# Optimization experiments

Measured on AMD Instinct MI355X. Metric: run time of the kernel, lower is better.

## Reference

```python
import jax, jax.numpy as jnp
import numpy as np

N_NODES = 50000
N_EDGES = 800000
NFEAT, NHID, NHEAD, NCLASS = 512, 64, 8, 40
NEG_SLOPE = 0.2  # LeakyReLU alpha from __init__


def setup_inputs() -> dict:
    key = jax.random.key(0)
    ks = jax.random.split(key, 8)
    glorot = lambda k, shape: jax.random.normal(k, shape, jnp.float32) * (2.0 / (shape[-2] + shape[-1])) ** 0.5
    return {
        "x": jax.random.normal(ks[0], (N_NODES, NFEAT), jnp.float32),
        "edge_list": jax.random.randint(ks[1], (2, N_EDGES), 0, N_NODES, jnp.int32),
        # nhead input-layer GATconv params: weight [H, nfeat, nhid], att [H, 2*nhid], bias [H, nhid]
        "W1": glorot(ks[2], (NHEAD, NFEAT, NHID)),
        "a1": jax.random.normal(ks[3], (NHEAD, 2 * NHID), jnp.float32) * 0.1,
        "b1": jnp.zeros((NHEAD, NHID), jnp.float32),
        # single output-head GATconv: [nhid*nhead, nclass]
        "W2": glorot(ks[4], (NHEAD * NHID, NCLASS)),
        "a2": jax.random.normal(ks[5], (2 * NCLASS,), jnp.float32) * 0.1,
        "b2": jnp.zeros((NCLASS,), jnp.float32),
    }


def _gat_layer(x, W, a, b, src, dst, n_nodes):
    """One GATconv head (eval mode, dropout = identity)."""
    h = x @ W                                  # [N, F]
    f = W.shape[-1]
    s_src = h @ a[:f]                          # [N] per-node src score
    s_dst = h @ a[f:]                          # [N] per-node dst score
    e = jax.nn.leaky_relu(s_src[src] + s_dst[dst], NEG_SLOPE)  # [E]
    # segment softmax over incoming edges of each dst node (numerically stable)
    m = jax.ops.segment_max(e, dst, num_segments=n_nodes)
    m = jax.lax.stop_gradient(jnp.where(jnp.isfinite(m), m, 0.0))
    w = jnp.exp(e - m[dst])
    denom = jax.ops.segment_sum(w, dst, num_segments=n_nodes)
    alpha = w / jnp.maximum(denom[dst], 1e-16)                 # [E]
    out = jax.ops.segment_sum(alpha[:, None] * h[src], dst, num_segments=n_nodes)
    return out + b


def reference(x, edge_list, W1, a1, b1, W2, a2, b2):
    n = x.shape[0]
    src, dst = edge_list[0], edge_list[1]
    # multi-head input layer, concat along feature dim
    heads = jax.vmap(lambda W, a, b: _gat_layer(x, W, a, b, src, dst, n))(W1, a1, b1)  # [H, N, nhid]
    h = jax.nn.elu(jnp.transpose(heads, (1, 0, 2)).reshape(n, -1))                      # [N, H*nhid]
    # single output head (mean over nhead_out=1)
    out = _gat_layer(h, W2, a2, b2, src, dst, n)                                        # [N, nclass]
    return jax.nn.log_softmax(out, axis=1)
```

## Files before the change

### kernel.cpp

```cpp
#include <hip/hip_runtime.h>
#include <math.h>

#define N_NODES 50000
#define N_EDGES 800000
#define NFEAT 512
#define NHID 64
#define NHEAD 8
#define NCLASS 40
#define NEG_SLOPE 0.2f

#define N_RT 3125
#define N_RT_PAD 3128
#define SCAN_NBLK 49

typedef __attribute__((ext_vector_type(8))) short short8;
typedef __attribute__((ext_vector_type(4))) short short4v;
typedef __attribute__((ext_vector_type(4))) float f32x4;

__device__ __forceinline__ float bf2f(short s) {
    return __uint_as_float(((unsigned)(unsigned short)s) << 16);
}
__device__ __forceinline__ short f2bf(float f) {
    unsigned u = __float_as_uint(f);
    unsigned r = (u + 0x7FFFu + ((u >> 16) & 1u)) >> 16;
    return (short)(unsigned short)r;
}



__global__ void count_deg(const int* __restrict__ el, int* __restrict__ deg) {
    int e = blockIdx.x * blockDim.x + threadIdx.x;
    if (e < N_EDGES) atomicAdd(&deg[el[N_EDGES + e]], 1);
}

__global__ __launch_bounds__(256) void scan1(const int* __restrict__ deg,
                                             int* __restrict__ loc,
                                             int* __restrict__ bsum) {
    int tid = threadIdx.x, lane = tid & 63, w = tid >> 6;
    int base = blockIdx.x * 1024 + tid * 4;
    int d0 = (base + 0 < N_NODES) ? deg[base + 0] : 0;
    int d1 = (base + 1 < N_NODES) ? deg[base + 1] : 0;
    int d2 = (base + 2 < N_NODES) ? deg[base + 2] : 0;
    int d3 = (base + 3 < N_NODES) ? deg[base + 3] : 0;
    int s0 = d0, s1 = s0 + d1, s2 = s1 + d2, s3 = s2 + d3;
    int t = s3;
#pragma unroll
    for (int d = 1; d < 64; d <<= 1) {
        int u = __shfl_up(t, d);
        if (lane >= d) t += u;
    }
    __shared__ int wsum[4];
    if (lane == 63) wsum[w] = t;
    __syncthreads();
    int woff = 0;
#pragma unroll
    for (int j = 0; j < 4; ++j) woff += (j < w) ? wsum[j] : 0;
    int excl = woff + t - s3;
    if (base + 0 < N_NODES) loc[base + 0] = excl + s0;
    if (base + 1 < N_NODES) loc[base + 1] = excl + s1;
    if (base + 2 < N_NODES) loc[base + 2] = excl + s2;
    if (base + 3 < N_NODES) loc[base + 3] = excl + s3;
    if (tid == 255) bsum[blockIdx.x] = woff + t;
}

__global__ __launch_bounds__(256) void scan3(const int* __restrict__ deg,
                                             const int* __restrict__ loc,
                                             const int* __restrict__ bsum,
                                             int* __restrict__ ptr,
                                             int* __restrict__ cursor) {
    __shared__ int sOff;
    if (threadIdx.x < 64) {
        int lane = threadIdx.x;
        int v = (lane < SCAN_NBLK && lane < (int)blockIdx.x) ? bsum[lane] : 0;
#pragma unroll
        for (int m = 1; m < 64; m <<= 1) v += __shfl_xor(v, m);
        if (lane == 0) sOff = v;
    }
    __syncthreads();
    int off = sOff;
    int base = blockIdx.x * 1024 + threadIdx.x * 4;
    if (blockIdx.x == 0 && threadIdx.x == 0) ptr[0] = 0;
#pragma unroll
    for (int k = 0; k < 4; ++k) {
        int i = base + k;
        if (i < N_NODES) {
            int P = off + loc[i];
            ptr[i + 1] = P;
            cursor[i] = P - deg[i];
        }
    }
}

__global__ void scatter_k(const int* __restrict__ el, int* __restrict__ cursor,
                          int* __restrict__ esrc) {
    int e = blockIdx.x * blockDim.x + threadIdx.x;
    if (e >= N_EDGES) return;
    int dst = el[N_EDGES + e];
    int p = atomicAdd(&cursor[dst], 1);
    esrc[p] = el[e];
}

__global__ __launch_bounds__(256) void pack_w(const float* __restrict__ W1,
                                              const float* __restrict__ W2,
                                              short* __restrict__ Wp1,
                                              short* __restrict__ Wp2) {
    int t = blockIdx.x * 256 + threadIdx.x;
    if (t < 32768) {
        int l = t & 63, ct = (t >> 6) & 7, ks = (t >> 9) & 15, g = t >> 13;
        int c = g * 128 + ct * 16 + (l & 15);
        int head = c >> 6, f = c & 63;
        int k0 = ks * 32 + (l >> 4) * 8;
        short8 o;
#pragma unroll
        for (int j = 0; j < 8; ++j)
            o[j] = f2bf(W1[(size_t)head * NFEAT * NHID + (k0 + j) * NHID + f]);
        *(short8*)(Wp1 + (size_t)t * 8) = o;
    } else if (t < 32768 + 3072) {
        int u = t - 32768;
        int l = u & 63;
        int kc = u >> 6;
        int ct2 = kc % 3, ks = kc / 3;
        int col = ct2 * 16 + (l & 15);
        short8 o;
#pragma unroll
        for (int j = 0; j < 8; ++j) {
            int kp = ks * 32 + (l >> 4) * 8 + j;
            int head = kp >> 6, fp = kp & 63;
            int l15 = fp >> 2, ctp = fp & 3;
            int ct = ((head & 1) << 2) | ctp;
            int gg = head >> 1;
            int orig_k = gg * 128 + ct * 16 + l15;
            o[j] = (col < NCLASS) ? f2bf(W2[(size_t)orig_k * NCLASS + col]) : (short)0;
        }
        *(short8*)(Wp2 + (size_t)u * 8) = o;
    }
}

__global__ __launch_bounds__(256, 2) void gemm1(const float* __restrict__ x,
                                                const short* __restrict__ Wp1,
                                                const float* __restrict__ a1,
                                                short* __restrict__ h1p,
                                                float* __restrict__ s1s,
                                                float* __restrict__ s1d) {
    __shared__ short As[2 * 16 * 64 * 8];
    int w = threadIdx.x >> 6, l = threadIdx.x & 63;
    int g = w;
    int rt0 = blockIdx.x * 2;
    int row0 = rt0 * 16;

#pragma unroll
    for (int u = 0; u < 8; ++u) {
        int idx = threadIdx.x + u * 256;
        int rl = idx >> 6, cg = idx & 63;
        int row = row0 + rl;
        short8 o;
        if (row < N_NODES) {
            const float* p = x + (size_t)row * NFEAT + cg * 8;
            float4 v0 = *(const float4*)p;
            float4 v1 = *(const float4*)(p + 4);
            o[0] = f2bf(v0.x); o[1] = f2bf(v0.y); o[2] = f2bf(v0.z); o[3] = f2bf(v0.w);
            o[4] = f2bf(v1.x); o[5] = f2bf(v1.y); o[6] = f2bf(v1.z); o[7] = f2bf(v1.w);
        } else {
#pragma unroll
            for (int j = 0; j < 8; ++j) o[j] = 0;
        }
        int rtl = rl >> 4, rloc = rl & 15, ks = cg >> 2, sub = cg & 3;
        int lane = rloc + sub * 16;
        *(short8*)(As + (((rtl * 16 + ks) * 64) + lane) * 8) = o;
    }
    __syncthreads();

    f32x4 acc[2][8];
#pragma unroll
    for (int i = 0; i < 2; ++i)
#pragma unroll
        for (int ct = 0; ct < 8; ++ct) acc[i][ct] = (f32x4){0.f, 0.f, 0.f, 0.f};

    const short* bP = Wp1 + (size_t)g * 16 * 4096 + l * 8;
    short8 bc[8];
#pragma unroll
    for (int ct = 0; ct < 8; ++ct) bc[ct] = *(const short8*)(bP + ct * 512);

    for (int ks = 0; ks < 16; ++ks) {
        int kn = (ks < 15) ? ks + 1 : ks;
        short8 bn[8];
#pragma unroll
        for (int ct = 0; ct < 8; ++ct) bn[ct] = *(const short8*)(bP + kn * 4096 + ct * 512);
        short8 a0 = *(const short8*)(As + ((ks)*64 + l) * 8);
        short8 a1v = *(const short8*)(As + ((16 + ks) * 64 + l) * 8);
#pragma unroll
        for (int ct = 0; ct < 8; ++ct) {
            acc[0][ct] = __builtin_amdgcn_mfma_f32_16x16x32_bf16(a0, bc[ct], acc[0][ct], 0, 0, 0);
            acc[1][ct] = __builtin_amdgcn_mfma_f32_16x16x32_bf16(a1v, bc[ct], acc[1][ct], 0, 0, 0);
        }
#pragma unroll
        for (int ct = 0; ct < 8; ++ct) bc[ct] = bn[ct];
    }

    float avs[8], avd[8];
#pragma unroll
    for (int ct = 0; ct < 8; ++ct) {
        int head = 2 * g + (ct >> 2);
        int f = (ct & 3) * 16 + (l & 15);
        avs[ct] = a1[head * 128 + f];
        avd[ct] = a1[head * 128 + 64 + f];
    }
    int l15 = l & 15;
    int rbase = (l >> 4) * 4;
#pragma unroll
    for (int i = 0; i < 2; ++i)
#pragma unroll
        for (int r = 0; r < 4; ++r) {
            int row = (rt0 + i) * 16 + rbase + r;
            float ps0 = 0.f, pd0 = 0.f, ps1 = 0.f, pd1 = 0.f;
#pragma unroll
            for (int ct = 0; ct < 4; ++ct) {
                ps0 += acc[i][ct][r] * avs[ct];
                pd0 += acc[i][ct][r] * avd[ct];
            }
#pragma unroll
            for (int ct = 4; ct < 8; ++ct) {
                ps1 += acc[i][ct][r] * avs[ct];
                pd1 += acc[i][ct][r] * avd[ct];
            }
#pragma unroll
            for (int mask = 1; mask < 16; mask <<= 1) {
                ps0 += __shfl_xor(ps0, mask);
                pd0 += __shfl_xor(pd0, mask);
                ps1 += __shfl_xor(ps1, mask);
                pd1 += __shfl_xor(pd1, mask);
            }
            if (row < N_NODES) {
                if (l15 == 0) {
                    s1s[row * 8 + 2 * g]     = ps0;
                    s1d[row * 8 + 2 * g]     = pd0;
                    s1s[row * 8 + 2 * g + 1] = ps1;
                    s1d[row * 8 + 2 * g + 1] = pd1;
                }
                short4v o0, o1;
#pragma unroll
                for (int c = 0; c < 4; ++c) { o0[c] = f2bf(acc[i][c][r]); o1[c] = f2bf(acc[i][4 + c][r]); }
                size_t base = (size_t)row * 512 + g * 128 + l15 * 4;
                *(short4v*)(h1p + base) = o0;
                *(short4v*)(h1p + base + 64) = o1;
            }
        }
}

__global__ __launch_bounds__(256, 4) void att1(const int* __restrict__ ptr,
                                               const int* __restrict__ esrc,
                                               const float* __restrict__ s1s,
                                               const float* __restrict__ s1d,
                                               const short* __restrict__ h1p,
                                               const float* __restrict__ b1,
                                               short* __restrict__ hcat) {
    int n = blockIdx.x * 4 + (threadIdx.x >> 6);
    int l = threadIdx.x & 63;
    if (n >= N_NODES) return;
    int beg = ptr[n], end = ptr[n + 1];
    int h = l >> 3;
    float sd = s1d[n * 8 + h];
    float den = 0.f;
    float acc[8] = {0.f, 0.f, 0.f, 0.f, 0.f, 0.f, 0.f, 0.f};
    const short* hb = h1p + l * 8;
    if (beg < end) {
        int last = end - 1;
        int p1 = (beg + 1 <= last) ? beg + 1 : last;
        int p2 = (beg + 2 <= last) ? beg + 2 : last;
        int p3 = (beg + 3 <= last) ? beg + 3 : last;
        int s0 = esrc[beg], s1 = esrc[p1], s2 = esrc[p2], s3 = esrc[p3];
        short8 v0 = *(const short8*)(hb + (size_t)s0 * 512);
        short8 v1 = *(const short8*)(hb + (size_t)s1 * 512);
        short8 v2 = *(const short8*)(hb + (size_t)s2 * 512);
        short8 v3 = *(const short8*)(hb + (size_t)s3 * 512);
        float ss0 = s1s[s0 * 8 + h], ss1 = s1s[s1 * 8 + h];
        float ss2 = s1s[s2 * 8 + h], ss3 = s1s[s3 * 8 + h];
        for (int i = beg; i < end; i += 4) {
            int ni = i + 4;
            int t0 = s0, t1 = s1, t2 = s2, t3 = s3;
            short8 u0 = v0, u1 = v1, u2 = v2, u3 = v3;
            float ts0 = ss0, ts1 = ss1, ts2 = ss2, ts3 = ss3;
            if (ni < end) {
                int q1 = (ni + 1 <= last) ? ni + 1 : last;
                int q2 = (ni + 2 <= last) ? ni + 2 : last;
                int q3 = (ni + 3 <= last) ? ni + 3 : last;
                t0 = esrc[ni]; t1 = esrc[q1]; t2 = esrc[q2]; t3 = esrc[q3];
                u0 = *(const short8*)(hb + (size_t)t0 * 512);
                u1 = *(const short8*)(hb + (size_t)t1 * 512);
                u2 = *(const short8*)(hb + (size_t)t2 * 512);
                u3 = *(const short8*)(hb + (size_t)t3 * 512);
                ts0 = s1s[t0 * 8 + h]; ts1 = s1s[t1 * 8 + h];
                ts2 = s1s[t2 * 8 + h]; ts3 = s1s[t3 * 8 + h];
            }
            float e0 = ss0 + sd, e1 = ss1 + sd, e2 = ss2 + sd, e3 = ss3 + sd;
            e0 = fmaxf(e0, NEG_SLOPE * e0);
            e1 = fmaxf(e1, NEG_SLOPE * e1);
            e2 = fmaxf(e2, NEG_SLOPE * e2);
            e3 = fmaxf(e3, NEG_SLOPE * e3);
            float w0 = __expf(e0);
            float w1 = (i + 1 < end) ? __expf(e1) : 0.f;
            float w2 = (i + 2 < end) ? __expf(e2) : 0.f;
            float w3 = (i + 3 < end) ? __expf(e3) : 0.f;
            den += (w0 + w1) + (w2 + w3);
#pragma unroll
            for (int j = 0; j < 8; ++j)
                acc[j] += (w0 * bf2f(v0[j]) + w1 * bf2f(v1[j])) +
                          (w2 * bf2f(v2[j]) + w3 * bf2f(v3[j]));
            s0 = t0; s1 = t1; s2 = t2; s3 = t3;
            v0 = u0; v1 = u1; v2 = u2; v3 = u3;
            ss0 = ts0; ss1 = ts1; ss2 = ts2; ss3 = ts3;
        }
    }
    float rden = 1.f / fmaxf(den, 1e-16f);
    short8 o;
#pragma unroll
    for (int j = 0; j < 8; ++j) {
        int forig = (j & 3) * 16 + (l & 7) * 2 + (j >> 2);
        float v = acc[j] * rden + b1[h * 64 + forig];
        v = v > 0.f ? v : (__expf(v) - 1.f);
        o[j] = f2bf(v);
    }
    *(short8*)(hcat + (size_t)n * 512 + l * 8) = o;
}

__global__ __launch_bounds__(256) void gemm2(const short* __restrict__ hcat,
                                             const short* __restrict__ Wp2,
                                             const float* __restrict__ a2,
                                             short* __restrict__ h2,
                                             float* __restrict__ s2s,
                                             float* __restrict__ s2d) {
    int w = threadIdx.x >> 6, l = threadIdx.x & 63;
    int rt = blockIdx.x * 4 + w;
    int arow = rt * 16 + (l & 15);
    const short* aBase = hcat + (size_t)arow * 512 + (l >> 4) * 8;
    f32x4 acc[3];
#pragma unroll
    for (int ct = 0; ct < 3; ++ct) acc[ct] = (f32x4){0.f, 0.f, 0.f, 0.f};
#pragma unroll 2
    for (int ks = 0; ks < 16; ++ks) {
        short8 a = *(const short8*)(aBase + ks * 32);
        const short* bp = Wp2 + (size_t)(ks * 3) * 512 + l * 8;
#pragma unroll
        for (int ct = 0; ct < 3; ++ct) {
            short8 b = *(const short8*)(bp + ct * 512);
            acc[ct] = __builtin_amdgcn_mfma_f32_16x16x32_bf16(a, b, acc[ct], 0, 0, 0);
        }
    }
    float ps[4] = {0.f, 0.f, 0.f, 0.f}, pd[4] = {0.f, 0.f, 0.f, 0.f};
    int cl = l & 15, rb = (l >> 4) * 4;
#pragma unroll
    for (int ct = 0; ct < 3; ++ct) {
        int col = ct * 16 + cl;
        if (col < NCLASS) {
#pragma unroll
            for (int r = 0; r < 4; ++r) {
                ps[r] += acc[ct][r] * a2[col];
                pd[r] += acc[ct][r] * a2[NCLASS + col];
                int row = rt * 16 + rb + r;
                if (row < N_NODES) h2[(size_t)row * NCLASS + col] = f2bf(acc[ct][r]);
            }
        }
    }
#pragma unroll
    for (int mask = 1; mask < 16; mask <<= 1)
#pragma unroll
        for (int r = 0; r < 4; ++r) {
            ps[r] += __shfl_xor(ps[r], mask);
            pd[r] += __shfl_xor(pd[r], mask);
        }
    if (cl == 0) {
#pragma unroll
        for (int r = 0; r < 4; ++r) {
            int row = rt * 16 + rb + r;
            if (row < N_NODES) { s2s[row] = ps[r]; s2d[row] = pd[r]; }
        }
    }
}

__global__ __launch_bounds__(256, 4) void att2(const int* __restrict__ ptr,
                                               const int* __restrict__ esrc,
                                               const float* __restrict__ s2s,
                                               const float* __restrict__ s2d,
                                               const short* __restrict__ h2,
                                               const float* __restrict__ b2,
                                               float* __restrict__ out) {
    int n = blockIdx.x * 4 + (threadIdx.x >> 6);
    int l = threadIdx.x & 63;
    if (n >= N_NODES) return;
    int beg = ptr[n], end = ptr[n + 1];
    float sd = s2d[n];
    float den = 0.f, acc = 0.f;
    int last = end - 1;
    bool act = (l < NCLASS);
    for (int i = beg; i < end; i += 4) {
        int i1 = (i + 1 <= last) ? i + 1 : last;
        int i2 = (i + 2 <= last) ? i + 2 : last;
        int i3 = (i + 3 <= last) ? i + 3 : last;
        int s0 = esrc[i], s1 = esrc[i1], s2 = esrc[i2], s3 = esrc[i3];
        float h0 = act ? bf2f(h2[(size_t)s0 * NCLASS + l]) : 0.f;
        float h1 = act ? bf2f(h2[(size_t)s1 * NCLASS + l]) : 0.f;
        float hh2 = act ? bf2f(h2[(size_t)s2 * NCLASS + l]) : 0.f;
        float h3 = act ? bf2f(h2[(size_t)s3 * NCLASS + l]) : 0.f;
        float e0 = s2s[s0] + sd;
        float e1 = s2s[s1] + sd;
        float e2 = s2s[s2] + sd;
        float e3 = s2s[s3] + sd;
        e0 = fmaxf(e0, NEG_SLOPE * e0);
        e1 = fmaxf(e1, NEG_SLOPE * e1);
        e2 = fmaxf(e2, NEG_SLOPE * e2);
        e3 = fmaxf(e3, NEG_SLOPE * e3);
        float w0 = __expf(e0);
        float w1 = (i + 1 < end) ? __expf(e1) : 0.f;
        float w2 = (i + 2 < end) ? __expf(e2) : 0.f;
        float w3 = (i + 3 < end) ? __expf(e3) : 0.f;
        den += (w0 + w1) + (w2 + w3);
        acc += (w0 * h0 + w1 * h1) + (w2 * hh2 + w3 * h3);
    }
    float v = act ? acc / fmaxf(den, 1e-16f) + b2[l] : -INFINITY;
    float mx = v;
#pragma unroll
    for (int o = 32; o; o >>= 1) mx = fmaxf(mx, __shfl_down(mx, o));
    mx = __shfl(mx, 0);
    float ex = act ? __expf(v - mx) : 0.f;
    float s = ex;
#pragma unroll
    for (int o = 32; o; o >>= 1) s += __shfl_down(s, o);
    s = __shfl(s, 0);
    float ls = __logf(s);
    if (act) out[(size_t)n * NCLASS + l] = v - mx - ls;
}


extern "C" void kernel_launch(void* const* d_in, const int* in_sizes, int n_in,
                              void* d_out, int out_size, void* d_ws, size_t ws_size,
                              hipStream_t stream) {
    const float* x  = (const float*)d_in[0];
    const int*   el = (const int*)d_in[1];
    const float* W1 = (const float*)d_in[2];
    const float* a1 = (const float*)d_in[3];
    const float* b1 = (const float*)d_in[4];
    const float* W2 = (const float*)d_in[5];
    const float* a2 = (const float*)d_in[6];
    const float* b2 = (const float*)d_in[7];
    float* out = (float*)d_out;

    short* sbase = (short*)d_ws;
    short* hcat  = sbase + 25624576;
    short* h1p   = sbase + 51249152;
    short* Wp1   = sbase + 76849152;
    short* Wp2   = sbase + 77111296;
    short* h2    = sbase + 77135872;
    float* fbase = (float*)(sbase + 79135872);
    float* s1s   = fbase;
    float* s1d   = fbase + 400000;
    float* s2s   = fbase + 800000;
    float* s2d   = fbase + 850000;
    int*   ibase = (int*)(fbase + 900000);
    int*   deg    = ibase;
    int*   ptr    = ibase + 50000;
    int*   cursor = ibase + 100001;
    int*   esrc   = ibase + 150001;
    int*   loc    = ibase + 950001;
    int*   bsum   = ibase + 1000001;

    hipMemsetAsync(deg, 0, (size_t)N_NODES * 4, stream);
    count_deg<<<(N_EDGES + 255) / 256, 256, 0, stream>>>(el, deg);
    scan1<<<SCAN_NBLK, 256, 0, stream>>>(deg, loc, bsum);
    scan3<<<SCAN_NBLK, 256, 0, stream>>>(deg, loc, bsum, ptr, cursor);
    scatter_k<<<(N_EDGES + 255) / 256, 256, 0, stream>>>(el, cursor, esrc);

    pack_w<<<140, 256, 0, stream>>>(W1, W2, Wp1, Wp2);

    gemm1<<<N_RT_PAD / 2, 256, 0, stream>>>(x, Wp1, a1, h1p, s1s, s1d);
    att1<<<(N_NODES + 3) / 4, 256, 0, stream>>>(ptr, esrc, s1s, s1d, h1p, b1, hcat);

    gemm2<<<N_RT_PAD / 4, 256, 0, stream>>>(hcat, Wp2, a2, h2, s2s, s2d);
    att2<<<(N_NODES + 3) / 4, 256, 0, stream>>>(ptr, esrc, s2s, s2d, h2, b2, out);
}
```

Measured before the change: 533.7 us.

## Deepen weight prefetch to two k-steps, swizzle LDS tile, nontemporal x loads

The first-layer projection GEMM now prefetches B fragments two k-steps ahead instead of one, processing k in pairs so more global loads are in flight across MFMAs. The LDS A-tile uses an XOR swizzle on slot indices to reduce bank conflicts on the short8 stores and loads. The x input is read with nontemporal loads since it is streamed once. The deeper prefetch doubles the B register footprint, which may raise VGPR pressure and lower occupancy.

```diff
diff --git a/kernel.cpp b/kernel.cpp
--- a/kernel.cpp
+++ b/kernel.cpp
@@ -25,6 +25,7 @@
     unsigned r = (u + 0x7FFFu + ((u >> 16) & 1u)) >> 16;
     return (short)(unsigned short)r;
 }
+__device__ __forceinline__ int swz(int s) { return s ^ ((s >> 4) & 7); }
 
 
 
@@ -156,17 +157,18 @@
         short8 o;
         if (row < N_NODES) {
             const float* p = x + (size_t)row * NFEAT + cg * 8;
-            float4 v0 = *(const float4*)p;
-            float4 v1 = *(const float4*)(p + 4);
-            o[0] = f2bf(v0.x); o[1] = f2bf(v0.y); o[2] = f2bf(v0.z); o[3] = f2bf(v0.w);
-            o[4] = f2bf(v1.x); o[5] = f2bf(v1.y); o[6] = f2bf(v1.z); o[7] = f2bf(v1.w);
+            f32x4 v0 = __builtin_nontemporal_load((const f32x4*)p);
+            f32x4 v1 = __builtin_nontemporal_load((const f32x4*)(p + 4));
+            o[0] = f2bf(v0[0]); o[1] = f2bf(v0[1]); o[2] = f2bf(v0[2]); o[3] = f2bf(v0[3]);
+            o[4] = f2bf(v1[0]); o[5] = f2bf(v1[1]); o[6] = f2bf(v1[2]); o[7] = f2bf(v1[3]);
         } else {
 #pragma unroll
             for (int j = 0; j < 8; ++j) o[j] = 0;
         }
         int rtl = rl >> 4, rloc = rl & 15, ks = cg >> 2, sub = cg & 3;
         int lane = rloc + sub * 16;
-        *(short8*)(As + (((rtl * 16 + ks) * 64) + lane) * 8) = o;
+        int slot = (rtl * 16 + ks) * 64 + lane;
+        *(short8*)(As + swz(slot) * 8) = o;
     }
     __syncthreads();
 
@@ -177,24 +179,37 @@
         for (int ct = 0; ct < 8; ++ct) acc[i][ct] = (f32x4){0.f, 0.f, 0.f, 0.f};
 
     const short* bP = Wp1 + (size_t)g * 16 * 4096 + l * 8;
-    short8 bc[8];
-#pragma unroll
-    for (int ct = 0; ct < 8; ++ct) bc[ct] = *(const short8*)(bP + ct * 512);
-
-    for (int ks = 0; ks < 16; ++ks) {
-        int kn = (ks < 15) ? ks + 1 : ks;
-        short8 bn[8];
-#pragma unroll
-        for (int ct = 0; ct < 8; ++ct) bn[ct] = *(const short8*)(bP + kn * 4096 + ct * 512);
-        short8 a0 = *(const short8*)(As + ((ks)*64 + l) * 8);
-        short8 a1v = *(const short8*)(As + ((16 + ks) * 64 + l) * 8);
+    short8 b0[8], b1[8], n0[8], n1[8];
+#pragma unroll
+    for (int ct = 0; ct < 8; ++ct) b0[ct] = *(const short8*)(bP + ct * 512);
+#pragma unroll
+    for (int ct = 0; ct < 8; ++ct) b1[ct] = *(const short8*)(bP + 4096 + ct * 512);
+
+    for (int kk = 0; kk < 8; ++kk) {
+        int ks0 = 2 * kk, ks1 = 2 * kk + 1;
+        int kp0 = (ks0 + 2 < 16) ? ks0 + 2 : 15;
+        int kp1 = (ks1 + 2 < 16) ? ks1 + 2 : 15;
+#pragma unroll
+        for (int ct = 0; ct < 8; ++ct) n0[ct] = *(const short8*)(bP + kp0 * 4096 + ct * 512);
+#pragma unroll
+        for (int ct = 0; ct < 8; ++ct) n1[ct] = *(const short8*)(bP + kp1 * 4096 + ct * 512);
+
+        short8 a00 = *(const short8*)(As + swz(ks0 * 64 + l) * 8);
+        short8 a01 = *(const short8*)(As + swz((16 + ks0) * 64 + l) * 8);
 #pragma unroll
         for (int ct = 0; ct < 8; ++ct) {
-            acc[0][ct] = __builtin_amdgcn_mfma_f32_16x16x32_bf16(a0, bc[ct], acc[0][ct], 0, 0, 0);
-            acc[1][ct] = __builtin_amdgcn_mfma_f32_16x16x32_bf16(a1v, bc[ct], acc[1][ct], 0, 0, 0);
-        }
-#pragma unroll
-        for (int ct = 0; ct < 8; ++ct) bc[ct] = bn[ct];
+            acc[0][ct] = __builtin_amdgcn_mfma_f32_16x16x32_bf16(a00, b0[ct], acc[0][ct], 0, 0, 0);
+            acc[1][ct] = __builtin_amdgcn_mfma_f32_16x16x32_bf16(a01, b0[ct], acc[1][ct], 0, 0, 0);
+        }
+        short8 a10 = *(const short8*)(As + swz(ks1 * 64 + l) * 8);
+        short8 a11 = *(const short8*)(As + swz((16 + ks1) * 64 + l) * 8);
+#pragma unroll
+        for (int ct = 0; ct < 8; ++ct) {
+            acc[0][ct] = __builtin_amdgcn_mfma_f32_16x16x32_bf16(a10, b1[ct], acc[0][ct], 0, 0, 0);
+            acc[1][ct] = __builtin_amdgcn_mfma_f32_16x16x32_bf16(a11, b1[ct], acc[1][ct], 0, 0, 0);
+        }
+#pragma unroll
+        for (int ct = 0; ct < 8; ++ct) { b0[ct] = n0[ct]; b1[ct] = n1[ct]; }
     }
 
     float avs[8], avd[8];
```

Measured after the change: 522.6 us. 1.02x faster.

## Fold attention vectors into W1 as extra GEMM column tile, enlarge gemm1 row tile

Applied to the files above, without the earlier changes.

Precomputes W1·a_src and W1·a_dst per head and packs them as a ninth 16-wide column tile, so gemm1 produces the attention scores directly from the MFMA instead of doing a shuffle-reduction epilogue. gemm1 also now processes 4 row tiles per block instead of 2, applies an XOR swizzle to the LDS A layout, and uses nontemporal loads for x. The B-operand prefetch double-buffering is removed in favor of unroll 2. The scores are now computed from bf16-rounded projected weights, which slightly changes numerics, and the larger accumulator array raises register pressure.

```diff
diff --git a/kernel.cpp b/kernel.cpp
--- a/kernel.cpp
+++ b/kernel.cpp
@@ -12,6 +12,7 @@
 #define N_RT 3125
 #define N_RT_PAD 3128
 #define SCAN_NBLK 49
+#define RT_BLK 4
 
 typedef __attribute__((ext_vector_type(8))) short short8;
 typedef __attribute__((ext_vector_type(4))) short short4v;
@@ -25,6 +26,7 @@
     unsigned r = (u + 0x7FFFu + ((u >> 16) & 1u)) >> 16;
     return (short)(unsigned short)r;
 }
+__device__ __forceinline__ int swz(int s) { return s ^ ((s >> 4) & 7); }
 
 
 
@@ -102,21 +104,45 @@
 
 __global__ __launch_bounds__(256) void pack_w(const float* __restrict__ W1,
                                               const float* __restrict__ W2,
-                                              short* __restrict__ Wp1,
+                                              const float* __restrict__ a1,
+                                              short* __restrict__ Wp1a,
                                               short* __restrict__ Wp2) {
     int t = blockIdx.x * 256 + threadIdx.x;
-    if (t < 32768) {
-        int l = t & 63, ct = (t >> 6) & 7, ks = (t >> 9) & 15, g = t >> 13;
-        int c = g * 128 + ct * 16 + (l & 15);
-        int head = c >> 6, f = c & 63;
-        int k0 = ks * 32 + (l >> 4) * 8;
+    if (t < 36864) {
+        int l = t & 63;
+        int idx = t >> 6;
+        int ct = idx % 9;
+        int ksg = idx / 9;
+        int ks = ksg & 15, g = ksg >> 4;
         short8 o;
-#pragma unroll
-        for (int j = 0; j < 8; ++j)
-            o[j] = f2bf(W1[(size_t)head * NFEAT * NHID + (k0 + j) * NHID + f]);
-        *(short8*)(Wp1 + (size_t)t * 8) = o;
-    } else if (t < 32768 + 3072) {
-        int u = t - 32768;
+        if (ct < 8) {
+            int c = g * 128 + ct * 16 + (l & 15);
+            int head = c >> 6, f = c & 63;
+            int k0 = ks * 32 + (l >> 4) * 8;
+#pragma unroll
+            for (int j = 0; j < 8; ++j)
+                o[j] = f2bf(W1[(size_t)head * NFEAT * NHID + (k0 + j) * NHID + f]);
+        } else {
+            int col = l & 15;
+            int k0 = ks * 32 + (l >> 4) * 8;
+#pragma unroll
+            for (int j = 0; j < 8; ++j) o[j] = 0;
+            if (col < 4) {
+                int head = 2 * g + (col >> 1);
+                const float* av = a1 + head * 128 + (col & 1) * 64;
+                const float* wb = W1 + (size_t)head * NFEAT * NHID;
+#pragma unroll
+                for (int j = 0; j < 8; ++j) {
+                    const float* wr = wb + (size_t)(k0 + j) * NHID;
+                    float s = 0.f;
+                    for (int f = 0; f < NHID; ++f) s += wr[f] * av[f];
+                    o[j] = f2bf(s);
+                }
+            }
+        }
+        *(short8*)(Wp1a + (size_t)t * 8) = o;
+    } else if (t < 36864 + 3072) {
+        int u = t - 36864;
         int l = u & 63;
         int kc = u >> 6;
         int ct2 = kc % 3, ks = kc / 3;
@@ -137,112 +163,80 @@
 }
 
 __global__ __launch_bounds__(256, 2) void gemm1(const float* __restrict__ x,
-                                                const short* __restrict__ Wp1,
-                                                const float* __restrict__ a1,
+                                                const short* __restrict__ Wp1a,
                                                 short* __restrict__ h1p,
                                                 float* __restrict__ s1s,
                                                 float* __restrict__ s1d) {
-    __shared__ short As[2 * 16 * 64 * 8];
+    __shared__ short As[RT_BLK * 16 * 64 * 8];
     int w = threadIdx.x >> 6, l = threadIdx.x & 63;
     int g = w;
-    int rt0 = blockIdx.x * 2;
+    int rt0 = blockIdx.x * RT_BLK;
     int row0 = rt0 * 16;
 
 #pragma unroll
-    for (int u = 0; u < 8; ++u) {
+    for (int u = 0; u < 4 * RT_BLK; ++u) {
         int idx = threadIdx.x + u * 256;
         int rl = idx >> 6, cg = idx & 63;
         int row = row0 + rl;
         short8 o;
         if (row < N_NODES) {
             const float* p = x + (size_t)row * NFEAT + cg * 8;
-            float4 v0 = *(const float4*)p;
-            float4 v1 = *(const float4*)(p + 4);
-            o[0] = f2bf(v0.x); o[1] = f2bf(v0.y); o[2] = f2bf(v0.z); o[3] = f2bf(v0.w);
-            o[4] = f2bf(v1.x); o[5] = f2bf(v1.y); o[6] = f2bf(v1.z); o[7] = f2bf(v1.w);
+            f32x4 v0 = __builtin_nontemporal_load((const f32x4*)p);
+            f32x4 v1 = __builtin_nontemporal_load((const f32x4*)(p + 4));
+            o[0] = f2bf(v0[0]); o[1] = f2bf(v0[1]); o[2] = f2bf(v0[2]); o[3] = f2bf(v0[3]);
+            o[4] = f2bf(v1[0]); o[5] = f2bf(v1[1]); o[6] = f2bf(v1[2]); o[7] = f2bf(v1[3]);
         } else {
 #pragma unroll
             for (int j = 0; j < 8; ++j) o[j] = 0;
         }
         int rtl = rl >> 4, rloc = rl & 15, ks = cg >> 2, sub = cg & 3;
-        int lane = rloc + sub * 16;
-        *(short8*)(As + (((rtl * 16 + ks) * 64) + lane) * 8) = o;
+        int slot = (rtl * 16 + ks) * 64 + rloc + sub * 16;
+        *(short8*)(As + swz(slot) * 8) = o;
     }
     __syncthreads();
 
-    f32x4 acc[2][8];
-#pragma unroll
-    for (int i = 0; i < 2; ++i)
-#pragma unroll
-        for (int ct = 0; ct < 8; ++ct) acc[i][ct] = (f32x4){0.f, 0.f, 0.f, 0.f};
-
-    const short* bP = Wp1 + (size_t)g * 16 * 4096 + l * 8;
-    short8 bc[8];
-#pragma unroll
-    for (int ct = 0; ct < 8; ++ct) bc[ct] = *(const short8*)(bP + ct * 512);
-
+    f32x4 acc[RT_BLK][9];
+#pragma unroll
+    for (int i = 0; i < RT_BLK; ++i)
+#pragma unroll
+        for (int ct = 0; ct < 9; ++ct) acc[i][ct] = (f32x4){0.f, 0.f, 0.f, 0.f};
+
+    const short* bP = Wp1a + (size_t)g * (16 * 9 * 512) + l * 8;
+#pragma unroll 2
     for (int ks = 0; ks < 16; ++ks) {
-        int kn = (ks < 15) ? ks + 1 : ks;
-        short8 bn[8];
-#pragma unroll
-        for (int ct = 0; ct < 8; ++ct) bn[ct] = *(const short8*)(bP + kn * 4096 + ct * 512);
-        short8 a0 = *(const short8*)(As + ((ks)*64 + l) * 8);
-        short8 a1v = *(const short8*)(As + ((16 + ks) * 64 + l) * 8);
-#pragma unroll
-        for (int ct = 0; ct < 8; ++ct) {
-            acc[0][ct] = __builtin_amdgcn_mfma_f32_16x16x32_bf16(a0, bc[ct], acc[0][ct], 0, 0, 0);
-            acc[1][ct] = __builtin_amdgcn_mfma_f32_16x16x32_bf16(a1v, bc[ct], acc[1][ct], 0, 0, 0);
-        }
-#pragma unroll
-        for (int ct = 0; ct < 8; ++ct) bc[ct] = bn[ct];
-    }
-
-    float avs[8], avd[8];
-#pragma unroll
-    for (int ct = 0; ct < 8; ++ct) {
-        int head = 2 * g + (ct >> 2);
-        int f = (ct & 3) * 16 + (l & 15);
-        avs[ct] = a1[head * 128 + f];
-        avd[ct] = a1[head * 128 + 64 + f];
-    }
+        short8 b[9];
+#pragma unroll
+        for (int ct = 0; ct < 9; ++ct) b[ct] = *(const short8*)(bP + ks * 4608 + ct * 512);
+        short8 a[RT_BLK];
+#pragma unroll
+        for (int i = 0; i < RT_BLK; ++i)
+            a[i] = *(const short8*)(As + swz((i * 16 + ks) * 64 + l) * 8);
+#pragma unroll
+        for (int i = 0; i < RT_BLK; ++i)
+#pragma unroll
+            for (int ct = 0; ct < 9; ++ct)
+                acc[i][ct] = __builtin_amdgcn_mfma_f32_16x16x32_bf16(a[i], b[ct], acc[i][ct], 0, 0, 0);
+    }
+
     int l15 = l & 15;
     int rbase = (l >> 4) * 4;
 #pragma unroll
-    for (int i = 0; i < 2; ++i)
+    for (int i = 0; i < RT_BLK; ++i)
 #pragma unroll
         for (int r = 0; r < 4; ++r) {
             int row = (rt0 + i) * 16 + rbase + r;
-            float ps0 = 0.f, pd0 = 0.f, ps1 = 0.f, pd1 = 0.f;
-#pragma unroll
-            for (int ct = 0; ct < 4; ++ct) {
-                ps0 += acc[i][ct][r] * avs[ct];
-                pd0 += acc[i][ct][r] * avd[ct];
-            }
-#pragma unroll
-            for (int ct = 4; ct < 8; ++ct) {
-                ps1 += acc[i][ct][r] * avs[ct];
-                pd1 += acc[i][ct][r] * avd[ct];
-            }
-#pragma unroll
-            for (int mask = 1; mask < 16; mask <<= 1) {
-                ps0 += __shfl_xor(ps0, mask);
-                pd0 += __shfl_xor(pd0, mask);
-                ps1 += __shfl_xor(ps1, mask);
-                pd1 += __shfl_xor(pd1, mask);
-            }
             if (row < N_NODES) {
-                if (l15 == 0) {
-                    s1s[row * 8 + 2 * g]     = ps0;
-                    s1d[row * 8 + 2 * g]     = pd0;
-                    s1s[row * 8 + 2 * g + 1] = ps1;
-                    s1d[row * 8 + 2 * g + 1] = pd1;
-                }
                 short4v o0, o1;
 #pragma unroll
                 for (int c = 0; c < 4; ++c) { o0[c] = f2bf(acc[i][c][r]); o1[c] = f2bf(acc[i][4 + c][r]); }
                 size_t base = (size_t)row * 512 + g * 128 + l15 * 4;
                 *(short4v*)(h1p + base) = o0;
                 *(short4v*)(h1p + base + 64) = o1;
+                float sv = acc[i][8][r];
+                if (l15 == 0)      s1s[row * 8 + 2 * g]     = sv;
+                else if (l15 == 1) s1d[row * 8 + 2 * g]     = sv;
+                else if (l15 == 2) s1s[row * 8 + 2 * g + 1] = sv;
+                else if (l15 == 3) s1d[row * 8 + 2 * g + 1] = sv;
             }
         }
 }
@@ -445,9 +439,9 @@
     float* out = (float*)d_out;
 
     short* sbase = (short*)d_ws;
+    short* Wp1a  = sbase;
     short* hcat  = sbase + 25624576;
     short* h1p   = sbase + 51249152;
-    short* Wp1   = sbase + 76849152;
     short* Wp2   = sbase + 77111296;
     short* h2    = sbase + 77135872;
     float* fbase = (float*)(sbase + 79135872);
@@ -469,9 +463,9 @@
     scan3<<<SCAN_NBLK, 256, 0, stream>>>(deg, loc, bsum, ptr, cursor);
     scatter_k<<<(N_EDGES + 255) / 256, 256, 0, stream>>>(el, cursor, esrc);
 
-    pack_w<<<140, 256, 0, stream>>>(W1, W2, Wp1, Wp2);
-
-    gemm1<<<N_RT_PAD / 2, 256, 0, stream>>>(x, Wp1, a1, h1p, s1s, s1d);
+    pack_w<<<156, 256, 0, stream>>>(W1, W2, a1, Wp1a, Wp2);
+
+    gemm1<<<N_RT_PAD / RT_BLK, 256, 0, stream>>>(x, Wp1a, h1p, s1s, s1d);
     att1<<<(N_NODES + 3) / 4, 256, 0, stream>>>(ptr, esrc, s1s, s1d, h1p, b1, hcat);
 
     gemm2<<<N_RT_PAD / 4, 256, 0, stream>>>(hcat, Wp2, a2, h2, s2s, s2d);
```

Result: faster. 504.9 us (-5.4%).
